# Kernel optimization log

Hardware: AMD Instinct MI355X
Metric: run time of the kernel (lower is better)

Reference implementation:

```python
import jax, jax.numpy as jnp
import numpy as np

NUM_EXPERTS = 8
CAP_FACTOR = 1.0
MIN_CAPACITY = 4


def setup_inputs() -> dict:
    key = jax.random.key(0)
    k0, k1, k2, k3 = jax.random.split(key, 4)
    H, F, E = 2048, 8192, NUM_EXPERTS
    hidden_states = jax.random.normal(k0, (4, 2048, H), dtype=jnp.float32)
    wg = jax.random.normal(k1, (H, E), dtype=jnp.float32) * 0.02
    w1 = jax.random.normal(k2, (E, H, F), dtype=jnp.float32) * 0.02
    b1 = jnp.zeros((E, F), dtype=jnp.float32)
    w2 = jax.random.normal(k3, (E, F, H), dtype=jnp.float32) * 0.02
    b2 = jnp.zeros((E, H), dtype=jnp.float32)
    return {"hidden_states": hidden_states, "wg": wg, "w1": w1, "b1": b1,
            "w2": w2, "b2": b2}


def reference(hidden_states, wg, w1, b1, w2, b2):
    E = NUM_EXPERTS
    M = hidden_states.shape[-1]
    x = hidden_states.reshape(-1, M)                     # [S, M] tokens
    S = x.shape[0]
    capacity = max(int(np.ceil(S / E * CAP_FACTOR)), MIN_CAPACITY)  # static

    # --- top-1 gating (DeepSpeed top1gating, fp32) ---
    logits = x.astype(jnp.float32) @ wg                  # [S, E]
    gates = jax.nn.softmax(logits, axis=-1)              # [S, E]
    idx1 = jnp.argmax(gates, axis=1)                     # [S]
    mask1 = jax.nn.one_hot(idx1, E, dtype=jnp.int32)     # [S, E]

    # load-balancing aux loss and per-expert counts
    me = jnp.mean(gates, axis=0)
    ce = jnp.mean(mask1.astype(jnp.float32), axis=0)
    l_aux = jnp.sum(me * ce) * E
    exp_counts = jnp.sum(mask1, axis=0)                  # [E]

    # capacity enforcement (use_rts=False -> keep earliest tokens per expert)
    locations1 = jnp.cumsum(mask1, axis=0) - 1           # [S, E] slot index
    mask1 = mask1 * (locations1 < capacity).astype(jnp.int32)
    mask1f = mask1.astype(gates.dtype)
    gates = gates * mask1f                               # zero dropped/other experts
    locs_s = jnp.sum(locations1 * mask1, axis=1)         # [S] slot of each token
    locs_sc = jax.nn.one_hot(locs_s, capacity, dtype=gates.dtype)  # [S, C]

    # combine / dispatch tensors
    combine = jnp.einsum('se,sc->sec', gates, locs_sc)   # [S, E, C]
    dispatch = (combine > 0).astype(x.dtype)             # bool mask as float

    # dispatch -> grouped expert MLP -> combine
    dispatched = jnp.einsum('sec,sm->ecm', dispatch, x)  # [E, C, M]
    h = jax.nn.gelu(jnp.einsum('ecm,emf->ecf', dispatched, w1) + b1[:, None, :])
    expert_out = jnp.einsum('ecf,efm->ecm', h, w2) + b2[:, None, :]
    out = jnp.einsum('sec,ecm->sm', combine.astype(x.dtype), expert_out)

    return out.reshape(hidden_states.shape), l_aux, exp_counts
```

## Files before the change

### kernel.cpp

```cpp
#include <hip/hip_runtime.h>
#include <stdint.h>

#define E_ 8
#define S_ 8192
#define H_ 2048
#define F_ 8192
#define C_ 1024
#define OUTN (S_*H_)

typedef __bf16 bf16x8 __attribute__((ext_vector_type(8)));
typedef float  f32x4  __attribute__((ext_vector_type(4)));
typedef unsigned short us8 __attribute__((ext_vector_type(8)));

__device__ __forceinline__ unsigned short f2bf(float f) {
    union { float f; unsigned u; } v; v.f = f;
    unsigned r = (v.u + 0x7FFFu + ((v.u >> 16) & 1u)) >> 16;
    return (unsigned short)r;
}

__device__ __forceinline__ void gload16(const void* g, void* l) {
    auto gp = (const __attribute__((address_space(1))) void*)(unsigned long long)(uintptr_t)g;
    auto lp = (__attribute__((address_space(3))) void*)(unsigned int)(uintptr_t)l;
    __builtin_amdgcn_global_load_lds(gp, lp, 16, 0, 0);
}

#define SB() __builtin_amdgcn_sched_barrier(0)
#define BAR() do { SB(); __builtin_amdgcn_s_barrier(); SB(); } while(0)

__global__ void zero_kernel(float* __restrict__ o, int n) {
    int i = blockIdx.x * blockDim.x + threadIdx.x;
    int st = gridDim.x * blockDim.x;
    for (; i < n; i += st) o[i] = 0.f;
}

__global__ __launch_bounds__(256)
void transpose_cvt(const float* __restrict__ src, unsigned short* __restrict__ dst,
                   int R, int Cc)
{
    __shared__ float t[64][65];
    int tilesR = R >> 6, tilesC = Cc >> 6;
    int per_e = tilesR * tilesC;
    int bid = blockIdx.x;
    int e  = bid / per_e;
    int rm = bid - e * per_e;
    int tc = rm / tilesR;
    int tr = rm - tc * tilesR;

    const float* s = src + (size_t)e * R * Cc + (size_t)(tr * 64) * Cc + tc * 64;
    int tid = threadIdx.x;
    int rr = tid >> 4;
    int cc = (tid & 15) << 2;
#pragma unroll
    for (int i = 0; i < 4; i++) {
        float4 v = *(const float4*)(s + (size_t)(rr + i * 16) * Cc + cc);
        t[rr + i * 16][cc + 0] = v.x;
        t[rr + i * 16][cc + 1] = v.y;
        t[rr + i * 16][cc + 2] = v.z;
        t[rr + i * 16][cc + 3] = v.w;
    }
    __syncthreads();
    int nl = tid >> 2;
    int kq = (tid & 3) << 4;
    us8 o0, o1;
#pragma unroll
    for (int i = 0; i < 8; i++) o0[i] = f2bf(t[kq + i][nl]);
#pragma unroll
    for (int i = 0; i < 8; i++) o1[i] = f2bf(t[kq + 8 + i][nl]);
    unsigned short* d = dst + (size_t)e * R * Cc + (size_t)(tc * 64 + nl) * R + tr * 64 + kq;
    *reinterpret_cast<us8*>(d)     = o0;
    *reinterpret_cast<us8*>(d + 8) = o1;
}

__global__ __launch_bounds__(256)
void gating_kernel(const float* __restrict__ x, const float* __restrict__ wg,
                   int* __restrict__ expert_id, float* __restrict__ gate_tok,
                   float* __restrict__ gates_all)
{
    int lane = threadIdx.x & 63;
    int wid  = threadIdx.x >> 6;
    int s = blockIdx.x * 4 + wid;
    const float* xs = x + (size_t)s * H_;
    float p[8];
#pragma unroll
    for (int j = 0; j < 8; j++) p[j] = 0.f;
    for (int h = lane; h < H_; h += 64) {
        float xv = xs[h];
        const float4* w4 = (const float4*)(wg + (size_t)h * 8);
        float4 a = w4[0], b = w4[1];
        p[0] += xv * a.x; p[1] += xv * a.y; p[2] += xv * a.z; p[3] += xv * a.w;
        p[4] += xv * b.x; p[5] += xv * b.y; p[6] += xv * b.z; p[7] += xv * b.w;
    }
#pragma unroll
    for (int off = 32; off; off >>= 1) {
#pragma unroll
        for (int j = 0; j < 8; j++) p[j] += __shfl_xor(p[j], off);
    }
    if (lane == 0) {
        float mx = p[0];
#pragma unroll
        for (int j = 1; j < 8; j++) mx = fmaxf(mx, p[j]);
        float ex[8], sum = 0.f;
#pragma unroll
        for (int j = 0; j < 8; j++) { ex[j] = expf(p[j] - mx); sum += ex[j]; }
        float inv = 1.f / sum;
        int am = 0; float best = p[0];
#pragma unroll
        for (int j = 1; j < 8; j++) if (p[j] > best) { best = p[j]; am = j; }
        expert_id[s] = am;
        gate_tok[s]  = expf(best - mx) * inv;
        float* ga = gates_all + (size_t)s * 8;
#pragma unroll
        for (int j = 0; j < 8; j++) ga[j] = ex[j] * inv;
    }
}

__global__ __launch_bounds__(1024)
void scan_kernel(const int* __restrict__ expert_id,
                 const float* __restrict__ gate_tok,
                 const float* __restrict__ gates_all,
                 int* __restrict__ token_slot,
                 float* __restrict__ gate_slot,
                 float* __restrict__ out_tail)
{
    __shared__ unsigned long long wt0[16], wt1[16];
    __shared__ unsigned long long tot0s, tot1s;
    __shared__ float red[1024 * 8];

    int tid = threadIdx.x;
    for (int i = tid; i < E_ * C_; i += 1024) token_slot[i] = -1;

    int ids[8];
#pragma unroll
    for (int j = 0; j < 8; j++) ids[j] = expert_id[tid * 8 + j];

    unsigned long long c0 = 0, c1 = 0;
#pragma unroll
    for (int j = 0; j < 8; j++) {
        int e = ids[j];
        unsigned long long inc = 1ull << ((e & 3) * 16);
        if (e < 4) c0 += inc; else c1 += inc;
    }
    unsigned long long s0 = c0, s1 = c1;
    int lane = tid & 63, w = tid >> 6;
#pragma unroll
    for (int off = 1; off < 64; off <<= 1) {
        unsigned long long t0 = __shfl_up(s0, off);
        unsigned long long t1 = __shfl_up(s1, off);
        if (lane >= off) { s0 += t0; s1 += t1; }
    }
    if (lane == 63) { wt0[w] = s0; wt1[w] = s1; }
    __syncthreads();
    unsigned long long off0 = 0, off1 = 0;
    for (int i = 0; i < w; i++) { off0 += wt0[i]; off1 += wt1[i]; }
    unsigned long long p0 = off0 + s0 - c0;
    unsigned long long p1 = off1 + s1 - c1;

#pragma unroll
    for (int j = 0; j < 8; j++) {
        int stok = tid * 8 + j;
        int e = ids[j];
        int sh = (e & 3) * 16;
        int slot = (int)(((e < 4 ? p0 : p1) >> sh) & 0xFFFFull);
        if (slot < C_) {
            token_slot[e * C_ + slot] = stok;
            gate_slot[e * C_ + slot]  = gate_tok[stok];
        }
        if (e < 4) p0 += 1ull << sh; else p1 += 1ull << sh;
    }
    if (tid == 1023) { tot0s = off0 + s0; tot1s = off1 + s1; }

    float me[8];
#pragma unroll
    for (int e2 = 0; e2 < 8; e2++) me[e2] = 0.f;
#pragma unroll
    for (int j = 0; j < 8; j++) {
        const float* ga = gates_all + (size_t)(tid * 8 + j) * 8;
#pragma unroll
        for (int e2 = 0; e2 < 8; e2++) me[e2] += ga[e2];
    }
#pragma unroll
    for (int e2 = 0; e2 < 8; e2++) red[tid * 8 + e2] = me[e2];
    __syncthreads();
    for (int st = 512; st > 0; st >>= 1) {
        if (tid < st) {
#pragma unroll
            for (int e2 = 0; e2 < 8; e2++) red[tid * 8 + e2] += red[(tid + st) * 8 + e2];
        }
        __syncthreads();
    }
    if (tid == 0) {
        float laux = 0.f;
#pragma unroll
        for (int e2 = 0; e2 < 8; e2++) {
            unsigned long long tv = (e2 < 4) ? tot0s : tot1s;
            float cnt = (float)((tv >> ((e2 & 3) * 16)) & 0xFFFFull);
            laux += red[e2] * cnt;
            out_tail[1 + e2] = cnt;
        }
        out_tail[0] = laux * (8.f / (8192.f * 8192.f));
    }
}

__global__ __launch_bounds__(256)
void gather_kernel(const float* __restrict__ x, const int* __restrict__ token_slot,
                   unsigned short* __restrict__ disp)
{
    int slot = blockIdx.x;
    int tok = token_slot[slot];
    int t = threadIdx.x;
    us8* d = reinterpret_cast<us8*>(disp + (size_t)slot * H_ + t * 8);
    if (tok < 0) {
        us8 z;
#pragma unroll
        for (int i = 0; i < 8; i++) z[i] = 0;
        *d = z;
        return;
    }
    const float4* s4 = (const float4*)(x + (size_t)tok * H_ + t * 8);
    float4 a = s4[0], b = s4[1];
    us8 o;
    o[0] = f2bf(a.x); o[1] = f2bf(a.y); o[2] = f2bf(a.z); o[3] = f2bf(a.w);
    o[4] = f2bf(b.x); o[5] = f2bf(b.y); o[6] = f2bf(b.z); o[7] = f2bf(b.w);
    *d = o;
}

template<int EPI, int K, int N>
__global__ __launch_bounds__(512, 2)
void gemm8p(const unsigned short* __restrict__ A,
            const unsigned short* __restrict__ B,
            const float* __restrict__ bias,
            unsigned short* __restrict__ hout,
            float* __restrict__ fout,
            const int* __restrict__ token_slot,
            const float* __restrict__ gate_slot,
            int Mt, int Nt)
{
    __shared__ char lds[131072];
    constexpr int KB   = K * 2;
    constexpr int HALF = 128 * KB;
    constexpr int NTI  = K / 64;

    int nwg = gridDim.x;
    int bid = blockIdx.x;
    int cpx = nwg >> 3;
    int wg  = (bid & 7) * cpx + (bid >> 3);
    int per_e = Mt * Nt;
    int e  = wg / per_e;
    int r  = wg - e * per_e;
    int nt = r / Mt;
    int mt = r - nt * Mt;

    int tid  = threadIdx.x;
    int lane = tid & 63;
    int wid  = tid >> 6;
    int wr = wid >> 2, wc = wid & 3;

    const char* Ag = (const char*)(A + ((size_t)e * 1024 + (size_t)mt * 256) * (size_t)K);
    const char* Bg = (const char*)(B + ((size_t)e * N    + (size_t)nt * 256) * (size_t)K);

    int r16s   = (tid >> 2) & 15;
    int scs    = ((tid & 3) * 16) ^ ((r16s & 8) << 2);
    int colblk = (tid >> 6) & 1;
    int rb0    = tid >> 7;
    int off0 = (rb0 * 16 + r16s) * KB + colblk * 64 + scs;
    int off1 = off0 + 64 * KB;
    int widb = wid * 1024;

    int lread = (lane & 15) * 64 + (((lane >> 4) * 16) ^ ((lane & 8) << 2));

    auto STAGE = [&](int ldsbase, const char* srcbase) {
        gload16(srcbase + off0, (char*)&lds[ldsbase + widb]);
        gload16(srcbase + off1, (char*)&lds[ldsbase + 8192 + widb]);
    };

    STAGE(65536,         Bg);
    STAGE(65536 + 16384, Bg + HALF);
    STAGE(0,             Ag);
    STAGE(16384,         Ag + HALF);
    STAGE(98304,         Bg + 128);
    STAGE(98304 + 16384, Bg + HALF + 128);
    STAGE(32768,         Ag + 128);
    SB(); asm volatile("s_waitcnt vmcnt(6)" ::: "memory"); SB();
    BAR();

    f32x4 acc[8][4];
    f32x4 zv = {0.f, 0.f, 0.f, 0.f};
#pragma unroll
    for (int i = 0; i < 8; i++)
#pragma unroll
        for (int j = 0; j < 4; j++) acc[i][j] = zv;

    int aoff_l = wr * 16384 + lread;
    int boff_l = 65536 + (wc >> 1) * 16384 + (wc & 1) * 8192 + lread;

    for (int t = 0; t < NTI; ++t) {
        int ab  = (t & 1) << 15;
        int nab = ab ^ 32768;
        const char* ald = lds + ab + aoff_l;
        const char* bld = lds + ab + boff_l;
        bf16x8 alo[4][2], ahi[4][2], blo[2][2], bhi[2][2];

#pragma unroll
        for (int mi = 0; mi < 4; mi++) {
            alo[mi][0] = *(const bf16x8*)(ald + mi * 2048);
            alo[mi][1] = *(const bf16x8*)(ald + mi * 2048 + 1024);
        }
#pragma unroll
        for (int ni = 0; ni < 2; ni++) {
            blo[ni][0] = *(const bf16x8*)(bld + ni * 2048);
            blo[ni][1] = *(const bf16x8*)(bld + ni * 2048 + 1024);
        }
        if (t + 1 < NTI) STAGE(nab + 16384, Ag + HALF + (size_t)(t + 1) * 128);
        BAR();
        __builtin_amdgcn_s_setprio(1);
#pragma unroll
        for (int mi = 0; mi < 4; mi++)
#pragma unroll
            for (int ni = 0; ni < 2; ni++) {
                acc[mi][ni] = __builtin_amdgcn_mfma_f32_16x16x32_bf16(alo[mi][0], blo[ni][0], acc[mi][ni], 0, 0, 0);
                acc[mi][ni] = __builtin_amdgcn_mfma_f32_16x16x32_bf16(alo[mi][1], blo[ni][1], acc[mi][ni], 0, 0, 0);
            }
        __builtin_amdgcn_s_setprio(0);
        BAR();

#pragma unroll
        for (int ni = 0; ni < 2; ni++) {
            bhi[ni][0] = *(const bf16x8*)(bld + 4096 + ni * 2048);
            bhi[ni][1] = *(const bf16x8*)(bld + 4096 + ni * 2048 + 1024);
        }
        BAR();
        __builtin_amdgcn_s_setprio(1);
#pragma unroll
        for (int mi = 0; mi < 4; mi++)
#pragma unroll
            for (int ni = 0; ni < 2; ni++) {
                acc[mi][ni + 2] = __builtin_amdgcn_mfma_f32_16x16x32_bf16(alo[mi][0], bhi[ni][0], acc[mi][ni + 2], 0, 0, 0);
                acc[mi][ni + 2] = __builtin_amdgcn_mfma_f32_16x16x32_bf16(alo[mi][1], bhi[ni][1], acc[mi][ni + 2], 0, 0, 0);
            }
        __builtin_amdgcn_s_setprio(0);
        BAR();

#pragma unroll
        for (int mi = 0; mi < 4; mi++) {
            ahi[mi][0] = *(const bf16x8*)(ald + 8192 + mi * 2048);
            ahi[mi][1] = *(const bf16x8*)(ald + 8192 + mi * 2048 + 1024);
        }
        if (t + 2 < NTI) {
            STAGE(ab + 65536,         Bg + (size_t)(t + 2) * 128);
            STAGE(ab + 65536 + 16384, Bg + HALF + (size_t)(t + 2) * 128);
        }
        BAR();
        __builtin_amdgcn_s_setprio(1);
#pragma unroll
        for (int mi = 0; mi < 4; mi++)
#pragma unroll
            for (int ni = 0; ni < 2; ni++) {
                acc[mi + 4][ni] = __builtin_amdgcn_mfma_f32_16x16x32_bf16(ahi[mi][0], blo[ni][0], acc[mi + 4][ni], 0, 0, 0);
                acc[mi + 4][ni] = __builtin_amdgcn_mfma_f32_16x16x32_bf16(ahi[mi][1], blo[ni][1], acc[mi + 4][ni], 0, 0, 0);
            }
        __builtin_amdgcn_s_setprio(0);
        BAR();

        if (t + 2 < NTI) STAGE(ab, Ag + (size_t)(t + 2) * 128);
        BAR();
        __builtin_amdgcn_s_setprio(1);
#pragma unroll
        for (int mi = 0; mi < 4; mi++)
#pragma unroll
            for (int ni = 0; ni < 2; ni++) {
                acc[mi + 4][ni + 2] = __builtin_amdgcn_mfma_f32_16x16x32_bf16(ahi[mi][0], bhi[ni][0], acc[mi + 4][ni + 2], 0, 0, 0);
                acc[mi + 4][ni + 2] = __builtin_amdgcn_mfma_f32_16x16x32_bf16(ahi[mi][1], bhi[ni][1], acc[mi + 4][ni + 2], 0, 0, 0);
            }
        __builtin_amdgcn_s_setprio(0);
        if (t + 2 < NTI) { SB(); asm volatile("s_waitcnt vmcnt(6)" ::: "memory"); SB(); }
        else             { SB(); asm volatile("s_waitcnt vmcnt(0)" ::: "memory"); SB(); }
        BAR();
    }

    int rbase = wr * 128 + (lane >> 4) * 4;
    int cbase = wc * 64 + (lane & 15);

    if (EPI == 0) {
        size_t rowg = (size_t)e * C_ + (size_t)mt * 256;
        float bb4[4];
#pragma unroll
        for (int ni = 0; ni < 4; ni++)
            bb4[ni] = bias[(size_t)e * N + nt * 256 + cbase + ni * 16];
#pragma unroll
        for (int mi = 0; mi < 8; mi++) {
#pragma unroll
            for (int rr2 = 0; rr2 < 4; rr2++) {
                int m = rbase + mi * 16 + rr2;
                size_t rb = (rowg + (size_t)m) * (size_t)N + nt * 256 + cbase;
#pragma unroll
                for (int ni = 0; ni < 4; ni++) {
                    float v = acc[mi][ni][rr2] + bb4[ni];
                    float u2 = 1.5957691216057308f * (v + 0.044715f * v * v * v);
                    float gl = v * __frcp_rn(1.f + __expf(-u2));
                    hout[rb + ni * 16] = f2bf(gl);
                }
            }
        }
    } else {
        float bb4[4];
#pragma unroll
        for (int ni = 0; ni < 4; ni++)
            bb4[ni] = bias[(size_t)e * N + nt * 256 + cbase + ni * 16];
#pragma unroll
        for (int mi = 0; mi < 8; mi++) {
#pragma unroll
            for (int rr2 = 0; rr2 < 4; rr2++) {
                int c = mt * 256 + rbase + mi * 16 + rr2;
                int tok = token_slot[e * C_ + c];
                if (tok < 0) continue;
                float g = gate_slot[e * C_ + c];
                size_t rb = (size_t)tok * (size_t)N + nt * 256 + cbase;
#pragma unroll
                for (int ni = 0; ni < 4; ni++) {
                    float v = (acc[mi][ni][rr2] + bb4[ni]) * g;
                    fout[rb + ni * 16] = v;
                }
            }
        }
    }
}

extern "C" void kernel_launch(void* const* d_in, const int* in_sizes, int n_in,
                              void* d_out, int out_size, void* d_ws, size_t ws_size,
                              hipStream_t stream)
{
    const float* x   = (const float*)d_in[0];
    const float* wgp = (const float*)d_in[1];
    const float* w1  = (const float*)d_in[2];
    const float* b1  = (const float*)d_in[3];
    const float* w2  = (const float*)d_in[4];
    const float* b2  = (const float*)d_in[5];
    float* out = (float*)d_out;

    char* ws = (char*)d_ws;
    unsigned short* w1t  = (unsigned short*)(ws);
    unsigned short* w2t  = (unsigned short*)(ws + 268435456ull);
    unsigned short* disp = (unsigned short*)(ws + 536870912ull);
    unsigned short* hbuf = (unsigned short*)(ws + 570425344ull);
    int*   expert_id  = (int*)  (ws + 704643072ull);
    float* gate_tok   = (float*)(ws + 704675840ull);
    float* gates_all  = (float*)(ws + 704708608ull);
    int*   token_slot = (int*)  (ws + 704970752ull);
    float* gate_slot  = (float*)(ws + 705003520ull);

    zero_kernel<<<4096, 256, 0, stream>>>(out, out_size);
    transpose_cvt<<<8 * 32 * 128, 256, 0, stream>>>(w1, w1t, 2048, 8192);
    transpose_cvt<<<8 * 128 * 32, 256, 0, stream>>>(w2, w2t, 8192, 2048);
    gating_kernel<<<2048, 256, 0, stream>>>(x, wgp, expert_id, gate_tok, gates_all);
    scan_kernel<<<1, 1024, 0, stream>>>(expert_id, gate_tok, gates_all, token_slot, gate_slot, out + OUTN);
    gather_kernel<<<8192, 256, 0, stream>>>(x, token_slot, disp);
    gemm8p<0, 2048, 8192><<<1024, 512, 0, stream>>>(disp, w1t, b1, hbuf, nullptr, nullptr, nullptr, 4, 32);
    gemm8p<1, 8192, 2048><<<256, 512, 0, stream>>>(hbuf, w2t, b2, nullptr, out, token_slot, gate_slot, 4, 8);
}
```

Baseline: 873.5 us.

## Restructure GEMM main loop into two phases with fewer barriers

```diff
diff --git a/kernel.cpp b/kernel.cpp
--- a/kernel.cpp
+++ b/kernel.cpp
@@ -226,18 +226,18 @@
 
 template<int EPI, int K, int N>
 __global__ __launch_bounds__(512, 2)
-void gemm8p(const unsigned short* __restrict__ A,
-            const unsigned short* __restrict__ B,
-            const float* __restrict__ bias,
-            unsigned short* __restrict__ hout,
-            float* __restrict__ fout,
-            const int* __restrict__ token_slot,
-            const float* __restrict__ gate_slot,
-            int Mt, int Nt)
-{
-    __shared__ char lds[131072];
+void gemm2sp(const unsigned short* __restrict__ A,
+             const unsigned short* __restrict__ B,
+             const float* __restrict__ bias,
+             unsigned short* __restrict__ hout,
+             float* __restrict__ fout,
+             const int* __restrict__ token_slot,
+             const float* __restrict__ gate_slot,
+             int Mt, int Nt)
+{
+    __shared__ uint4 shm[8192];
     constexpr int KB   = K * 2;
-    constexpr int HALF = 128 * KB;
+    constexpr int QG   = 64 * KB;
     constexpr int NTI  = K / 64;
 
     int nwg = gridDim.x;
@@ -263,23 +263,22 @@
     int colblk = (tid >> 6) & 1;
     int rb0    = tid >> 7;
     int off0 = (rb0 * 16 + r16s) * KB + colblk * 64 + scs;
-    int off1 = off0 + 64 * KB;
     int widb = wid * 1024;
 
     int lread = (lane & 15) * 64 + (((lane >> 4) * 16) ^ ((lane & 8) << 2));
 
-    auto STAGE = [&](int ldsbase, const char* srcbase) {
-        gload16(srcbase + off0, (char*)&lds[ldsbase + widb]);
-        gload16(srcbase + off1, (char*)&lds[ldsbase + 8192 + widb]);
+    auto SQ = [&](int dstbyte, const char* src) {
+        gload16(src + off0, (char*)shm + dstbyte + widb);
     };
 
-    STAGE(65536,         Bg);
-    STAGE(65536 + 16384, Bg + HALF);
-    STAGE(0,             Ag);
-    STAGE(16384,         Ag + HALF);
-    STAGE(98304,         Bg + 128);
-    STAGE(98304 + 16384, Bg + HALF + 128);
-    STAGE(32768,         Ag + 128);
+#pragma unroll
+    for (int j = 0; j < 4; j++) SQ(65536 + j * 8192, Bg + j * QG);
+#pragma unroll
+    for (int j = 0; j < 4; j++) SQ(j * 8192,         Ag + j * QG);
+#pragma unroll
+    for (int j = 0; j < 4; j++) SQ(98304 + j * 8192, Bg + j * QG + 128);
+    SQ(32768,         Ag + 0 * QG + 128);
+    SQ(32768 + 16384, Ag + 2 * QG + 128);
     SB(); asm volatile("s_waitcnt vmcnt(6)" ::: "memory"); SB();
     BAR();
 
@@ -296,84 +295,65 @@
     for (int t = 0; t < NTI; ++t) {
         int ab  = (t & 1) << 15;
         int nab = ab ^ 32768;
-        const char* ald = lds + ab + aoff_l;
-        const char* bld = lds + ab + boff_l;
-        bf16x8 alo[4][2], ahi[4][2], blo[2][2], bhi[2][2];
+        int abl = ab + aoff_l;
+        int bbl = ab + boff_l;
+        bf16x8 alo[4][2], ahi[4][2], bv[4][2];
 
 #pragma unroll
         for (int mi = 0; mi < 4; mi++) {
-            alo[mi][0] = *(const bf16x8*)(ald + mi * 2048);
-            alo[mi][1] = *(const bf16x8*)(ald + mi * 2048 + 1024);
+            alo[mi][0] = *(const bf16x8*)&shm[(abl + mi * 2048) >> 4];
+            alo[mi][1] = *(const bf16x8*)&shm[(abl + mi * 2048 + 1024) >> 4];
         }
 #pragma unroll
         for (int ni = 0; ni < 2; ni++) {
-            blo[ni][0] = *(const bf16x8*)(bld + ni * 2048);
-            blo[ni][1] = *(const bf16x8*)(bld + ni * 2048 + 1024);
-        }
-        if (t + 1 < NTI) STAGE(nab + 16384, Ag + HALF + (size_t)(t + 1) * 128);
+            bv[ni][0]     = *(const bf16x8*)&shm[(bbl + ni * 2048) >> 4];
+            bv[ni][1]     = *(const bf16x8*)&shm[(bbl + ni * 2048 + 1024) >> 4];
+            bv[ni + 2][0] = *(const bf16x8*)&shm[(bbl + 4096 + ni * 2048) >> 4];
+            bv[ni + 2][1] = *(const bf16x8*)&shm[(bbl + 4096 + ni * 2048 + 1024) >> 4];
+        }
+        if (t + 1 < NTI) {
+            SQ(nab + 8192,  Ag + 1 * QG + (size_t)(t + 1) * 128);
+            SQ(nab + 24576, Ag + 3 * QG + (size_t)(t + 1) * 128);
+        }
         BAR();
         __builtin_amdgcn_s_setprio(1);
 #pragma unroll
         for (int mi = 0; mi < 4; mi++)
 #pragma unroll
-            for (int ni = 0; ni < 2; ni++) {
-                acc[mi][ni] = __builtin_amdgcn_mfma_f32_16x16x32_bf16(alo[mi][0], blo[ni][0], acc[mi][ni], 0, 0, 0);
-                acc[mi][ni] = __builtin_amdgcn_mfma_f32_16x16x32_bf16(alo[mi][1], blo[ni][1], acc[mi][ni], 0, 0, 0);
+            for (int ni = 0; ni < 4; ni++) {
+                acc[mi][ni] = __builtin_amdgcn_mfma_f32_16x16x32_bf16(alo[mi][0], bv[ni][0], acc[mi][ni], 0, 0, 0);
+                acc[mi][ni] = __builtin_amdgcn_mfma_f32_16x16x32_bf16(alo[mi][1], bv[ni][1], acc[mi][ni], 0, 0, 0);
             }
         __builtin_amdgcn_s_setprio(0);
+        if (t < NTI - 1) { SB(); asm volatile("s_waitcnt vmcnt(8)" ::: "memory"); SB(); }
+        else             { SB(); asm volatile("s_waitcnt vmcnt(0)" ::: "memory"); SB(); }
         BAR();
 
 #pragma unroll
-        for (int ni = 0; ni < 2; ni++) {
-            bhi[ni][0] = *(const bf16x8*)(bld + 4096 + ni * 2048);
-            bhi[ni][1] = *(const bf16x8*)(bld + 4096 + ni * 2048 + 1024);
+        for (int mi = 0; mi < 4; mi++) {
+            ahi[mi][0] = *(const bf16x8*)&shm[(abl + 8192 + mi * 2048) >> 4];
+            ahi[mi][1] = *(const bf16x8*)&shm[(abl + 8192 + mi * 2048 + 1024) >> 4];
+        }
+        if (t + 2 < NTI) {
+#pragma unroll
+            for (int j = 0; j < 4; j++)
+                SQ(ab + 65536 + j * 8192, Bg + j * QG + (size_t)(t + 2) * 128);
+            SQ(ab,         Ag + 0 * QG + (size_t)(t + 2) * 128);
+            SQ(ab + 16384, Ag + 2 * QG + (size_t)(t + 2) * 128);
         }
         BAR();
         __builtin_amdgcn_s_setprio(1);
 #pragma unroll
         for (int mi = 0; mi < 4; mi++)
 #pragma unroll
-            for (int ni = 0; ni < 2; ni++) {
-                acc[mi][ni + 2] = __builtin_amdgcn_mfma_f32_16x16x32_bf16(alo[mi][0], bhi[ni][0], acc[mi][ni + 2], 0, 0, 0);
-                acc[mi][ni + 2] = __builtin_amdgcn_mfma_f32_16x16x32_bf16(alo[mi][1], bhi[ni][1], acc[mi][ni + 2], 0, 0, 0);
+            for (int ni = 0; ni < 4; ni++) {
+                acc[mi + 4][ni] = __builtin_amdgcn_mfma_f32_16x16x32_bf16(ahi[mi][0], bv[ni][0], acc[mi + 4][ni], 0, 0, 0);
+                acc[mi + 4][ni] = __builtin_amdgcn_mfma_f32_16x16x32_bf16(ahi[mi][1], bv[ni][1], acc[mi + 4][ni], 0, 0, 0);
             }
         __builtin_amdgcn_s_setprio(0);
-        BAR();
-
-#pragma unroll
-        for (int mi = 0; mi < 4; mi++) {
-            ahi[mi][0] = *(const bf16x8*)(ald + 8192 + mi * 2048);
-            ahi[mi][1] = *(const bf16x8*)(ald + 8192 + mi * 2048 + 1024);
-        }
-        if (t + 2 < NTI) {
-            STAGE(ab + 65536,         Bg + (size_t)(t + 2) * 128);
-            STAGE(ab + 65536 + 16384, Bg + HALF + (size_t)(t + 2) * 128);
-        }
-        BAR();
-        __builtin_amdgcn_s_setprio(1);
-#pragma unroll
-        for (int mi = 0; mi < 4; mi++)
-#pragma unroll
-            for (int ni = 0; ni < 2; ni++) {
-                acc[mi + 4][ni] = __builtin_amdgcn_mfma_f32_16x16x32_bf16(ahi[mi][0], blo[ni][0], acc[mi + 4][ni], 0, 0, 0);
-                acc[mi + 4][ni] = __builtin_amdgcn_mfma_f32_16x16x32_bf16(ahi[mi][1], blo[ni][1], acc[mi + 4][ni], 0, 0, 0);
-            }
-        __builtin_amdgcn_s_setprio(0);
-        BAR();
-
-        if (t + 2 < NTI) STAGE(ab, Ag + (size_t)(t + 2) * 128);
-        BAR();
-        __builtin_amdgcn_s_setprio(1);
-#pragma unroll
-        for (int mi = 0; mi < 4; mi++)
-#pragma unroll
-            for (int ni = 0; ni < 2; ni++) {
-                acc[mi + 4][ni + 2] = __builtin_amdgcn_mfma_f32_16x16x32_bf16(ahi[mi][0], bhi[ni][0], acc[mi + 4][ni + 2], 0, 0, 0);
-                acc[mi + 4][ni + 2] = __builtin_amdgcn_mfma_f32_16x16x32_bf16(ahi[mi][1], bhi[ni][1], acc[mi + 4][ni + 2], 0, 0, 0);
-            }
-        __builtin_amdgcn_s_setprio(0);
-        if (t + 2 < NTI) { SB(); asm volatile("s_waitcnt vmcnt(6)" ::: "memory"); SB(); }
-        else             { SB(); asm volatile("s_waitcnt vmcnt(0)" ::: "memory"); SB(); }
+        if      (t + 2 < NTI)  { SB(); asm volatile("s_waitcnt vmcnt(8)" ::: "memory"); SB(); }
+        else if (t == NTI - 2) { SB(); asm volatile("s_waitcnt vmcnt(2)" ::: "memory"); SB(); }
+        else                   { SB(); asm volatile("s_waitcnt vmcnt(0)" ::: "memory"); SB(); }
         BAR();
     }
 
@@ -454,6 +434,6 @@
     gating_kernel<<<2048, 256, 0, stream>>>(x, wgp, expert_id, gate_tok, gates_all);
     scan_kernel<<<1, 1024, 0, stream>>>(expert_id, gate_tok, gates_all, token_slot, gate_slot, out + OUTN);
     gather_kernel<<<8192, 256, 0, stream>>>(x, token_slot, disp);
-    gemm8p<0, 2048, 8192><<<1024, 512, 0, stream>>>(disp, w1t, b1, hbuf, nullptr, nullptr, nullptr, 4, 32);
-    gemm8p<1, 8192, 2048><<<256, 512, 0, stream>>>(hbuf, w2t, b2, nullptr, out, token_slot, gate_slot, 4, 8);
-}
+    gemm2sp<0, 2048, 8192><<<1024, 512, 0, stream>>>(disp, w1t, b1, hbuf, nullptr, nullptr, nullptr, 4, 32);
+    gemm2sp<1, 8192, 2048><<<256, 512, 0, stream>>>(hbuf, w2t, b2, nullptr, out, token_slot, gate_slot, 4, 8);
+}
```

New measurement: 923.3 us. 5.7% more time.
